# Kernel tuning notes

Hardware: AMD Instinct MI355X
Metric: run time of the kernel (lower is better)

## Reference

```python
import jax, jax.numpy as jnp
import numpy as np

GRID_SIZE = 5
SPLINE_ORDER = 3
HIDDEN = 128
IN_FT = 768
BATCH = 32768

def make_grid():
    # uniform grid on [-1, 1] extended by spline_order knots on each side
    h = 2.0 / GRID_SIZE
    return (jnp.arange(-SPLINE_ORDER, GRID_SIZE + SPLINE_ORDER + 1, dtype=jnp.float32) * h - 1.0)

def b_splines(x, grid):
    # x: (B, in) -> bases: (B, in, GRID_SIZE + SPLINE_ORDER) via Cox-de-Boor recursion
    xe = x[..., None]                                  # (B, in, 1)
    bases = ((xe >= grid[:-1]) & (xe < grid[1:])).astype(x.dtype)
    for k in range(1, SPLINE_ORDER + 1):
        left = (xe - grid[:-(k + 1)]) / (grid[k:-1] - grid[:-(k + 1)]) * bases[..., :-1]
        right = (grid[k + 1:] - xe) / (grid[k + 1:] - grid[1:-k]) * bases[..., 1:]
        bases = left + right
    return bases

def kan_layer(x, base_w, spline_w, grid):
    # base_w: (out, in); spline_w: (out, in, G+k)
    B = x.shape[0]
    base_out = jax.nn.silu(x) @ base_w.T
    bas = b_splines(x, grid).reshape(B, -1)            # (B, in*(G+k))
    spline_out = bas @ spline_w.reshape(spline_w.shape[0], -1).T
    return base_out + spline_out

def setup_inputs() -> dict:
    key = jax.random.key(0)
    ks = jax.random.split(key, 8)
    nb = GRID_SIZE + SPLINE_ORDER  # 8 basis functions per edge
    return {
        "stm": jax.random.uniform(ks[0], (BATCH, IN_FT), dtype=jnp.float32),
        "nstm": jax.random.uniform(ks[1], (BATCH, IN_FT), dtype=jnp.float32),
        "ft_w": jax.random.normal(ks[2], (HIDDEN, IN_FT), dtype=jnp.float32) * 0.02,
        "ft_b": jnp.zeros((HIDDEN,), dtype=jnp.float32),
        "kan1_base_w": jax.random.normal(ks[3], (HIDDEN, 2 * HIDDEN), dtype=jnp.float32) * 0.05,
        "kan1_spline_w": jax.random.normal(ks[4], (HIDDEN, 2 * HIDDEN, nb), dtype=jnp.float32) * 0.05,
        "kan2_base_w": jax.random.normal(ks[5], (1, HIDDEN), dtype=jnp.float32) * 0.05,
        "kan2_spline_w": jax.random.normal(ks[6], (1, HIDDEN, nb), dtype=jnp.float32) * 0.05,
    }

def reference(stm, nstm, ft_w, ft_b, kan1_base_w, kan1_spline_w, kan2_base_w, kan2_spline_w):
    grid = make_grid()
    stm_h = stm @ ft_w.T + ft_b
    nstm_h = nstm @ ft_w.T + ft_b
    hidden = jnp.concatenate([stm_h, nstm_h], axis=1)   # (B, 2*HIDDEN)
    hidden = kan_layer(hidden, kan1_base_w, kan1_spline_w, grid)
    out = kan_layer(hidden, kan2_base_w, kan2_spline_w, grid)
    return jax.nn.sigmoid(out)
```

## Files before the change

### kernel.cpp

```cpp
#include <hip/hip_runtime.h>
#include <hip/hip_bf16.h>
#include <math.h>
#include <stdint.h>

typedef __attribute__((ext_vector_type(8))) short bf16x8;
typedef __attribute__((ext_vector_type(4))) float f32x4;

__device__ __forceinline__ uint32_t pack2(float a, float b) {
    union { __hip_bfloat162 h2; uint32_t u; } c;
    c.h2 = __float22bfloat162_rn(make_float2(a, b));
    return c.u;
}
__device__ __forceinline__ unsigned short f2bf(float f) {
    union { __hip_bfloat16 h; unsigned short u; } c;
    c.h = __float2bfloat16(f);
    return c.u;
}
__device__ __forceinline__ float bf2f(unsigned short h) {
    union { uint32_t u; float f; } c; c.u = ((uint32_t)h) << 16;
    return c.f;
}
__device__ __forceinline__ float silu_f(float x) {
    return x / (1.0f + __expf(-x));
}

__device__ __forceinline__ void bspline8(float x, float* __restrict__ b) {
    const float tt = (x + 2.2f) * 2.5f;
#pragma unroll
    for (int v = 0; v < 8; ++v) {
        float y = fabsf(tt - (float)(v + 2));
        float p = fmaxf(2.0f - y, 0.0f);
        float q = fmaxf(1.0f - y, 0.0f);
        b[v] = (p * p * p - 4.0f * q * q * q) * (1.0f / 6.0f);
    }
}

__global__ __launch_bounds__(256) void prep_wbf(const float* __restrict__ ftw,
                                                unsigned short* __restrict__ WbF) {
    const int idx = blockIdx.x * 256 + threadIdx.x;
    const int e = idx & 7, l = (idx >> 3) & 63, ks = (idx >> 9) & 3;
    const int nt = (idx >> 11) & 1, wc = (idx >> 12) & 3, tile = idx >> 14;
    const int col = wc * 32 + nt * 16 + (l & 15);
    const int k = tile * 128 + ks * 32 + (l >> 4) * 8 + e;
    WbF[idx] = f2bf(ftw[(size_t)col * 768 + k]);
}

__global__ __launch_bounds__(256) void prep_bpf(const float* __restrict__ bw,
                                                const float* __restrict__ sw,
                                                unsigned short* __restrict__ BpF) {
    const int idx = blockIdx.x * 256 + threadIdx.x;
    const int e = idx & 7, l = (idx >> 3) & 63, ks = (idx >> 9) & 3;
    const int nt = (idx >> 11) & 1, wc = (idx >> 12) & 3, jb = idx >> 14;
    const int col = wc * 32 + nt * 16 + (l & 15);
    const int k = jb * 128 + ks * 32 + (l >> 4) * 8 + e;
    const int f = k >> 4, v = k & 15;
    float val = 0.f;
    if (v == 0) val = bw[col * 256 + f];
    else if (v <= 8) val = sw[(size_t)(col * 256 + f) * 8 + (v - 1)];
    BpF[idx] = f2bf(val);
}

__global__ __launch_bounds__(512, 4) void kan_fused(
        const float* __restrict__ stm, const float* __restrict__ nstm,
        const unsigned short* __restrict__ WbF, const float* __restrict__ bias,
        const unsigned short* __restrict__ BpF,
        const float* __restrict__ w2b, const float* __restrict__ w2s,
        float* __restrict__ out) {
    __shared__ alignas(16) char lds[65536];
    char* smA  = lds;
    char* phi1 = lds + 16384;
    char* smHT = lds + 32768;

    const int r0 = blockIdx.x * 64;
    const int t = threadIdx.x;
    const int l = t & 63, w = t >> 6;
    const int fr = l & 15, h = l >> 4;
    const int wr = w >> 2, wc = w & 3;

    const int arow = t >> 3;
    const int acol = (t & 7) * 16;
    const uint32_t adst0 = (uint32_t)arow * 256u +
        ((uint32_t)(((t & 7) * 2) ^ (arow & 15)) << 4);
    const uint32_t adst1 = (uint32_t)arow * 256u +
        ((uint32_t)(((t & 7) * 2 + 1) ^ (arow & 15)) << 4);

    f32x4 acc[2][2];
#pragma unroll
    for (int mt = 0; mt < 2; ++mt)
#pragma unroll
        for (int nt = 0; nt < 2; ++nt) acc[mt][nt] = (f32x4){0.f, 0.f, 0.f, 0.f};

    float4 regY[4], regZ[4];
    bf16x8 bf[2][4];

#define FT_ISSUE(REG, TK)                                                      \
    {                                                                          \
        const float* __restrict__ Ap = ((TK) >= 6) ? nstm : stm;               \
        const int kk = ((TK) % 6) * 128;                                       \
        _Pragma("unroll") for (int q = 0; q < 4; ++q)                          \
            REG[q] = *reinterpret_cast<const float4*>(                         \
                &Ap[(size_t)(r0 + arow) * 768 + kk + acol + q * 4]);           \
    }

#define FT_WRITE(REG)                                                          \
    {                                                                          \
        int4 w0, w1;                                                           \
        w0.x = (int)pack2(REG[0].x, REG[0].y);                                 \
        w0.y = (int)pack2(REG[0].z, REG[0].w);                                 \
        w0.z = (int)pack2(REG[1].x, REG[1].y);                                 \
        w0.w = (int)pack2(REG[1].z, REG[1].w);                                 \
        w1.x = (int)pack2(REG[2].x, REG[2].y);                                 \
        w1.y = (int)pack2(REG[2].z, REG[2].w);                                 \
        w1.z = (int)pack2(REG[3].x, REG[3].y);                                 \
        w1.w = (int)pack2(REG[3].z, REG[3].w);                                 \
        *reinterpret_cast<int4*>(smA + adst0) = w0;                            \
        *reinterpret_cast<int4*>(smA + adst1) = w1;                            \
    }

#define LOADF(PTR, TILE)                                                       \
    {                                                                          \
        const unsigned short* __restrict__ fb =                                \
            (PTR) + (size_t)(TILE) * 16384 + wc * 4096 + l * 8;                \
        _Pragma("unroll") for (int nt = 0; nt < 2; ++nt)                       \
            _Pragma("unroll") for (int ks = 0; ks < 4; ++ks)                   \
                bf[nt][ks] = *reinterpret_cast<const bf16x8*>(                 \
                    fb + nt * 2048 + ks * 512);                                \
    }

#define GEMM_STEP(PHI)                                                         \
    _Pragma("unroll") for (int ks = 0; ks < 4; ++ks) {                         \
        bf16x8 a[2];                                                           \
        _Pragma("unroll") for (int mt = 0; mt < 2; ++mt) {                     \
            const uint32_t row = (uint32_t)(wr * 32 + mt * 16 + fr);           \
            a[mt] = *reinterpret_cast<const bf16x8*>(                          \
                (PHI) + row * 256u +                                           \
                (((uint32_t)(ks * 4 + h) ^ (row & 15u)) << 4));                \
        }                                                                      \
        _Pragma("unroll") for (int mt = 0; mt < 2; ++mt)                       \
            _Pragma("unroll") for (int nt = 0; nt < 2; ++nt)                   \
                acc[mt][nt] = __builtin_amdgcn_mfma_f32_16x16x32_bf16(         \
                    a[mt], bf[nt][ks], acc[mt][nt], 0, 0, 0);                  \
    }

#define DUMP_H(SO)                                                             \
    _Pragma("unroll") for (int nt = 0; nt < 2; ++nt) {                         \
        const int col = wc * 32 + nt * 16 + fr;                                \
        const float bv = bias[col];                                            \
        const int feat = (SO) + col;                                           \
        _Pragma("unroll") for (int mt = 0; mt < 2; ++mt) {                     \
            const int rowb = wr * 32 + mt * 16 + h * 4;                        \
            int2 o;                                                            \
            o.x = (int)pack2(acc[mt][nt][0] + bv, acc[mt][nt][1] + bv);        \
            o.y = (int)pack2(acc[mt][nt][2] + bv, acc[mt][nt][3] + bv);        \
            const uint32_t db = (uint32_t)feat * 128u +                        \
                ((uint32_t)((rowb >> 3) ^ (feat & 7)) << 4) +                  \
                (uint32_t)(rowb & 7) * 2u;                                     \
            *reinterpret_cast<int2*>(smHT + db) = o;                           \
            acc[mt][nt] = (f32x4){0.f, 0.f, 0.f, 0.f};                         \
        }                                                                      \
    }

#define EXPAND(DST, JF)                                                        \
    {                                                                          \
        const int feat = (JF) * 8 + w;                                         \
        const unsigned short xv = *reinterpret_cast<const unsigned short*>(    \
            smHT + (uint32_t)feat * 128u +                                     \
            ((uint32_t)((l >> 3) ^ (feat & 7)) << 4) + (uint32_t)(l & 7) * 2u);\
        const float x = bf2f(xv);                                              \
        float bs[8];                                                           \
        bspline8(x, bs);                                                       \
        const uint32_t pw0 = pack2(silu_f(x), bs[0]);                          \
        const uint32_t pw1 = pack2(bs[1], bs[2]);                              \
        const uint32_t pw2 = pack2(bs[3], bs[4]);                              \
        const uint32_t pw3 = pack2(bs[5], bs[6]);                              \
        const uint32_t pw4 = pack2(bs[7], 0.f);                                \
        const uint32_t d0 = (uint32_t)l * 256u +                               \
            ((uint32_t)((2 * w) ^ (l & 15)) << 4);                             \
        const uint32_t d1 = (uint32_t)l * 256u +                               \
            ((uint32_t)((2 * w + 1) ^ (l & 15)) << 4);                         \
        *reinterpret_cast<int4*>((DST) + d0) =                                 \
            make_int4((int)pw0, (int)pw1, (int)pw2, (int)pw3);                 \
        *reinterpret_cast<int4*>((DST) + d1) = make_int4((int)pw4, 0, 0, 0);   \
    }

#define BAR1()                                                                 \
    asm volatile("s_waitcnt lgkmcnt(0)" ::: "memory");                         \
    __builtin_amdgcn_sched_barrier(0);                                         \
    __builtin_amdgcn_s_barrier();
#define BAR2()                                                                 \
    __builtin_amdgcn_sched_barrier(0);                                         \
    __builtin_amdgcn_s_barrier();                                              \
    __builtin_amdgcn_sched_barrier(0);

    FT_ISSUE(regY, 0);
    FT_ISSUE(regZ, 1);
#pragma unroll 1
    for (int pp = 0; pp < 6; ++pp) {
        FT_WRITE(regY);
        if (pp < 5) FT_ISSUE(regY, 2 * pp + 2);
        LOADF(WbF, (2 * pp) % 6);
        BAR1();
        __builtin_amdgcn_s_setprio(1);
        GEMM_STEP(smA);
        __builtin_amdgcn_s_setprio(0);
        BAR2();
        FT_WRITE(regZ);
        if (pp < 5) FT_ISSUE(regZ, 2 * pp + 3);
        LOADF(WbF, (2 * pp + 1) % 6);
        BAR1();
        __builtin_amdgcn_s_setprio(1);
        GEMM_STEP(smA);
        __builtin_amdgcn_s_setprio(0);
        if (pp == 2) { DUMP_H(0); }
        if (pp == 5) { DUMP_H(128); }
        asm volatile("s_waitcnt lgkmcnt(0)" ::: "memory");
        BAR2();
    }

    EXPAND(smA, 0);
#pragma unroll 1
    for (int jb = 0; jb < 32; ++jb) {
        char* phiC = (jb & 1) ? phi1 : smA;
        char* phiN = (jb & 1) ? smA : phi1;
        LOADF(BpF, jb);
        if (jb < 31) EXPAND(phiN, jb + 1);
        BAR1();
        __builtin_amdgcn_s_setprio(1);
        GEMM_STEP(phiC);
        __builtin_amdgcn_s_setprio(0);
        BAR2();
    }

    unsigned short* smH2 = (unsigned short*)lds;
#pragma unroll
    for (int mt = 0; mt < 2; ++mt)
#pragma unroll
        for (int nt = 0; nt < 2; ++nt) {
            const int col = wc * 32 + nt * 16 + fr;
#pragma unroll
            for (int j = 0; j < 4; ++j) {
                const int row = wr * 32 + mt * 16 + h * 4 + j;
                smH2[row * 136 + col] = f2bf(acc[mt][nt][j]);
            }
        }
    __syncthreads();
    const int row2 = t >> 3, qd = t & 7;
    float sum = 0.f;
#pragma unroll 4
    for (int i = 0; i < 16; ++i) {
        const int j = qd * 16 + ((i + qd * 2) & 15);
        const float x = bf2f(smH2[row2 * 136 + j]);
        float bs[8];
        bspline8(x, bs);
        const float4 s0 = *reinterpret_cast<const float4*>(&w2s[j * 8]);
        const float4 s1 = *reinterpret_cast<const float4*>(&w2s[j * 8 + 4]);
        float s = silu_f(x) * w2b[j];
        s += bs[0] * s0.x + bs[1] * s0.y + bs[2] * s0.z + bs[3] * s0.w;
        s += bs[4] * s1.x + bs[5] * s1.y + bs[6] * s1.z + bs[7] * s1.w;
        sum += s;
    }
    sum += __shfl_xor(sum, 1, 64);
    sum += __shfl_xor(sum, 2, 64);
    sum += __shfl_xor(sum, 4, 64);
    if (qd == 0) out[r0 + row2] = 1.0f / (1.0f + __expf(-sum));
}

extern "C" void kernel_launch(void* const* d_in, const int* in_sizes, int n_in,
                              void* d_out, int out_size, void* d_ws, size_t ws_size,
                              hipStream_t stream) {
    const float* stm  = (const float*)d_in[0];
    const float* nstm = (const float*)d_in[1];
    const float* ft_w = (const float*)d_in[2];
    const float* ft_b = (const float*)d_in[3];
    const float* k1bw = (const float*)d_in[4];
    const float* k1sw = (const float*)d_in[5];
    const float* k2bw = (const float*)d_in[6];
    const float* k2sw = (const float*)d_in[7];
    float* out = (float*)d_out;

    char* ws = (char*)d_ws;
    unsigned short* WbF = (unsigned short*)ws;
    unsigned short* BpF = (unsigned short*)(ws + 196608);

    prep_wbf<<<384, 256, 0, stream>>>(ft_w, WbF);
    prep_bpf<<<2048, 256, 0, stream>>>(k1bw, k1sw, BpF);
    kan_fused<<<512, 512, 0, stream>>>(stm, nstm, WbF, ft_b, BpF, k2bw, k2sw, out);
}
```

Measured before the change: 110.4 us.

## Warp-specialize fused KAN kernel into MFMA consumer and staging producer waves

The 8 waves are split into two roles. Four consumer waves each run a 32x64 output tile of MFMAs and prefetch the next weight fragments. Four producer waves stage the next A tile (bf16-converted input or B-spline expansion) into a double-buffered LDS slot. This replaces the old scheme in which all 8 waves alternated loading and computing, and aims to overlap global loads and spline expansion with matrix math using one barrier per step. The weight prep layouts are changed to match the 2x4 n-tiling. In exchange, half the waves now do no MFMA work, and each consumer needs more accumulator and fragment registers.

```diff
diff --git a/kernel.cpp b/kernel.cpp
--- a/kernel.cpp
+++ b/kernel.cpp
@@ -39,8 +39,8 @@
                                                 unsigned short* __restrict__ WbF) {
     const int idx = blockIdx.x * 256 + threadIdx.x;
     const int e = idx & 7, l = (idx >> 3) & 63, ks = (idx >> 9) & 3;
-    const int nt = (idx >> 11) & 1, wc = (idx >> 12) & 3, tile = idx >> 14;
-    const int col = wc * 32 + nt * 16 + (l & 15);
+    const int nt = (idx >> 11) & 3, wc = (idx >> 13) & 1, tile = idx >> 14;
+    const int col = wc * 64 + nt * 16 + (l & 15);
     const int k = tile * 128 + ks * 32 + (l >> 4) * 8 + e;
     WbF[idx] = f2bf(ftw[(size_t)col * 768 + k]);
 }
@@ -50,8 +50,8 @@
                                                 unsigned short* __restrict__ BpF) {
     const int idx = blockIdx.x * 256 + threadIdx.x;
     const int e = idx & 7, l = (idx >> 3) & 63, ks = (idx >> 9) & 3;
-    const int nt = (idx >> 11) & 1, wc = (idx >> 12) & 3, jb = idx >> 14;
-    const int col = wc * 32 + nt * 16 + (l & 15);
+    const int nt = (idx >> 11) & 3, wc = (idx >> 13) & 1, jb = idx >> 14;
+    const int col = wc * 64 + nt * 16 + (l & 15);
     const int k = jb * 128 + ks * 32 + (l >> 4) * 8 + e;
     const int f = k >> 4, v = k & 15;
     float val = 0.f;
@@ -67,84 +67,76 @@
         const float* __restrict__ w2b, const float* __restrict__ w2s,
         float* __restrict__ out) {
     __shared__ alignas(16) char lds[65536];
-    char* smA  = lds;
-    char* phi1 = lds + 16384;
+    char* buf0 = lds;
+    char* buf1 = lds + 16384;
     char* smHT = lds + 32768;
 
     const int r0 = blockIdx.x * 64;
     const int t = threadIdx.x;
     const int l = t & 63, w = t >> 6;
     const int fr = l & 15, h = l >> 4;
-    const int wr = w >> 2, wc = w & 3;
-
-    const int arow = t >> 3;
-    const int acol = (t & 7) * 16;
-    const uint32_t adst0 = (uint32_t)arow * 256u +
-        ((uint32_t)(((t & 7) * 2) ^ (arow & 15)) << 4);
-    const uint32_t adst1 = (uint32_t)arow * 256u +
-        ((uint32_t)(((t & 7) * 2 + 1) ^ (arow & 15)) << 4);
-
-    f32x4 acc[2][2];
+    const bool cons = (w < 4);
+    const int wr = (w >> 1) & 1, wc = w & 1;
+    const int p = w & 3;
+
+    f32x4 acc[2][4];
 #pragma unroll
     for (int mt = 0; mt < 2; ++mt)
 #pragma unroll
-        for (int nt = 0; nt < 2; ++nt) acc[mt][nt] = (f32x4){0.f, 0.f, 0.f, 0.f};
-
-    float4 regY[4], regZ[4];
-    bf16x8 bf[2][4];
-
-#define FT_ISSUE(REG, TK)                                                      \
-    {                                                                          \
-        const float* __restrict__ Ap = ((TK) >= 6) ? nstm : stm;               \
-        const int kk = ((TK) % 6) * 128;                                       \
-        _Pragma("unroll") for (int q = 0; q < 4; ++q)                          \
-            REG[q] = *reinterpret_cast<const float4*>(                         \
-                &Ap[(size_t)(r0 + arow) * 768 + kk + acol + q * 4]);           \
-    }
-
-#define FT_WRITE(REG)                                                          \
-    {                                                                          \
-        int4 w0, w1;                                                           \
-        w0.x = (int)pack2(REG[0].x, REG[0].y);                                 \
-        w0.y = (int)pack2(REG[0].z, REG[0].w);                                 \
-        w0.z = (int)pack2(REG[1].x, REG[1].y);                                 \
-        w0.w = (int)pack2(REG[1].z, REG[1].w);                                 \
-        w1.x = (int)pack2(REG[2].x, REG[2].y);                                 \
-        w1.y = (int)pack2(REG[2].z, REG[2].w);                                 \
-        w1.z = (int)pack2(REG[3].x, REG[3].y);                                 \
-        w1.w = (int)pack2(REG[3].z, REG[3].w);                                 \
-        *reinterpret_cast<int4*>(smA + adst0) = w0;                            \
-        *reinterpret_cast<int4*>(smA + adst1) = w1;                            \
-    }
+        for (int nt = 0; nt < 4; ++nt) acc[mt][nt] = (f32x4){0.f, 0.f, 0.f, 0.f};
+
+    bf16x8 bf[4][4];
 
 #define LOADF(PTR, TILE)                                                       \
     {                                                                          \
         const unsigned short* __restrict__ fb =                                \
-            (PTR) + (size_t)(TILE) * 16384 + wc * 4096 + l * 8;                \
-        _Pragma("unroll") for (int nt = 0; nt < 2; ++nt)                       \
+            (PTR) + (size_t)(TILE) * 16384 + wc * 8192 + l * 8;                \
+        _Pragma("unroll") for (int nt = 0; nt < 4; ++nt)                       \
             _Pragma("unroll") for (int ks = 0; ks < 4; ++ks)                   \
                 bf[nt][ks] = *reinterpret_cast<const bf16x8*>(                 \
                     fb + nt * 2048 + ks * 512);                                \
     }
 
-#define GEMM_STEP(PHI)                                                         \
+#define STAGE_A(DST, T)                                                        \
+    {                                                                          \
+        const float* __restrict__ Ap = ((T) >= 6) ? nstm : stm;                \
+        const int kk = ((T) % 6) * 128;                                        \
+        float4 fv[8];                                                          \
+        _Pragma("unroll") for (int i = 0; i < 8; ++i) {                        \
+            const int row = p * 16 + i * 2 + (l >> 5);                         \
+            fv[i] = *reinterpret_cast<const float4*>(                          \
+                &Ap[(size_t)(r0 + row) * 768 + kk + (l & 31) * 4]);            \
+        }                                                                      \
+        _Pragma("unroll") for (int i = 0; i < 8; ++i) {                        \
+            const int row = p * 16 + i * 2 + (l >> 5);                         \
+            const uint32_t c = (uint32_t)((l & 31) >> 1);                      \
+            const uint32_t dst = (uint32_t)row * 256u +                        \
+                ((c ^ (uint32_t)(row & 15)) << 4) + (uint32_t)(l & 1) * 8u;    \
+            int2 v;                                                            \
+            v.x = (int)pack2(fv[i].x, fv[i].y);                                \
+            v.y = (int)pack2(fv[i].z, fv[i].w);                                \
+            *reinterpret_cast<int2*>((DST) + dst) = v;                         \
+        }                                                                      \
+    }
+
+#define GEMM_STEP(SRC)                                                         \
     _Pragma("unroll") for (int ks = 0; ks < 4; ++ks) {                         \
         bf16x8 a[2];                                                           \
         _Pragma("unroll") for (int mt = 0; mt < 2; ++mt) {                     \
             const uint32_t row = (uint32_t)(wr * 32 + mt * 16 + fr);           \
             a[mt] = *reinterpret_cast<const bf16x8*>(                          \
-                (PHI) + row * 256u +                                           \
+                (SRC) + row * 256u +                                           \
                 (((uint32_t)(ks * 4 + h) ^ (row & 15u)) << 4));                \
         }                                                                      \
         _Pragma("unroll") for (int mt = 0; mt < 2; ++mt)                       \
-            _Pragma("unroll") for (int nt = 0; nt < 2; ++nt)                   \
+            _Pragma("unroll") for (int nt = 0; nt < 4; ++nt)                   \
                 acc[mt][nt] = __builtin_amdgcn_mfma_f32_16x16x32_bf16(         \
                     a[mt], bf[nt][ks], acc[mt][nt], 0, 0, 0);                  \
     }
 
 #define DUMP_H(SO)                                                             \
-    _Pragma("unroll") for (int nt = 0; nt < 2; ++nt) {                         \
-        const int col = wc * 32 + nt * 16 + fr;                                \
+    _Pragma("unroll") for (int nt = 0; nt < 4; ++nt) {                         \
+        const int col = wc * 64 + nt * 16 + fr;                                \
         const float bv = bias[col];                                            \
         const int feat = (SO) + col;                                           \
         _Pragma("unroll") for (int mt = 0; mt < 2; ++mt) {                     \
@@ -160,9 +152,10 @@
         }                                                                      \
     }
 
-#define EXPAND(DST, JF)                                                        \
-    {                                                                          \
-        const int feat = (JF) * 8 + w;                                         \
+#define EXPAND2(DST, JB)                                                       \
+    _Pragma("unroll") for (int e = 0; e < 2; ++e) {                            \
+        const int f = p * 2 + e;                                               \
+        const int feat = (JB) * 8 + f;                                         \
         const unsigned short xv = *reinterpret_cast<const unsigned short*>(    \
             smHT + (uint32_t)feat * 128u +                                     \
             ((uint32_t)((l >> 3) ^ (feat & 7)) << 4) + (uint32_t)(l & 7) * 2u);\
@@ -175,74 +168,72 @@
         const uint32_t pw3 = pack2(bs[5], bs[6]);                              \
         const uint32_t pw4 = pack2(bs[7], 0.f);                                \
         const uint32_t d0 = (uint32_t)l * 256u +                               \
-            ((uint32_t)((2 * w) ^ (l & 15)) << 4);                             \
+            ((uint32_t)((2 * f) ^ (l & 15)) << 4);                             \
         const uint32_t d1 = (uint32_t)l * 256u +                               \
-            ((uint32_t)((2 * w + 1) ^ (l & 15)) << 4);                         \
+            ((uint32_t)((2 * f + 1) ^ (l & 15)) << 4);                         \
         *reinterpret_cast<int4*>((DST) + d0) =                                 \
             make_int4((int)pw0, (int)pw1, (int)pw2, (int)pw3);                 \
         *reinterpret_cast<int4*>((DST) + d1) = make_int4((int)pw4, 0, 0, 0);   \
     }
 
-#define BAR1()                                                                 \
+#define PH_BAR()                                                               \
     asm volatile("s_waitcnt lgkmcnt(0)" ::: "memory");                         \
-    __builtin_amdgcn_sched_barrier(0);                                         \
-    __builtin_amdgcn_s_barrier();
-#define BAR2()                                                                 \
     __builtin_amdgcn_sched_barrier(0);                                         \
     __builtin_amdgcn_s_barrier();                                              \
     __builtin_amdgcn_sched_barrier(0);
 
-    FT_ISSUE(regY, 0);
-    FT_ISSUE(regZ, 1);
+    if (cons) { LOADF(WbF, 0); }
+    else      { STAGE_A(buf0, 0); }
+    PH_BAR();
 #pragma unroll 1
-    for (int pp = 0; pp < 6; ++pp) {
-        FT_WRITE(regY);
-        if (pp < 5) FT_ISSUE(regY, 2 * pp + 2);
-        LOADF(WbF, (2 * pp) % 6);
-        BAR1();
-        __builtin_amdgcn_s_setprio(1);
-        GEMM_STEP(smA);
-        __builtin_amdgcn_s_setprio(0);
-        BAR2();
-        FT_WRITE(regZ);
-        if (pp < 5) FT_ISSUE(regZ, 2 * pp + 3);
-        LOADF(WbF, (2 * pp + 1) % 6);
-        BAR1();
-        __builtin_amdgcn_s_setprio(1);
-        GEMM_STEP(smA);
-        __builtin_amdgcn_s_setprio(0);
-        if (pp == 2) { DUMP_H(0); }
-        if (pp == 5) { DUMP_H(128); }
-        asm volatile("s_waitcnt lgkmcnt(0)" ::: "memory");
-        BAR2();
-    }
-
-    EXPAND(smA, 0);
+    for (int tile = 0; tile < 12; ++tile) {
+        char* cur = (tile & 1) ? buf1 : buf0;
+        char* nxt = (tile & 1) ? buf0 : buf1;
+        if (cons) {
+            __builtin_amdgcn_s_setprio(1);
+            GEMM_STEP(cur);
+            __builtin_amdgcn_s_setprio(0);
+            if (tile < 11) { LOADF(WbF, (tile + 1) % 6); }
+            if (tile == 5) { DUMP_H(0); }
+            if (tile == 11) { DUMP_H(128); }
+        } else {
+            if (tile < 11) { STAGE_A(nxt, tile + 1); }
+        }
+        PH_BAR();
+    }
+
+    if (cons) { LOADF(BpF, 0); }
+    else      { EXPAND2(buf0, 0); }
+    PH_BAR();
 #pragma unroll 1
     for (int jb = 0; jb < 32; ++jb) {
-        char* phiC = (jb & 1) ? phi1 : smA;
-        char* phiN = (jb & 1) ? smA : phi1;
-        LOADF(BpF, jb);
-        if (jb < 31) EXPAND(phiN, jb + 1);
-        BAR1();
-        __builtin_amdgcn_s_setprio(1);
-        GEMM_STEP(phiC);
-        __builtin_amdgcn_s_setprio(0);
-        BAR2();
+        char* cur = (jb & 1) ? buf1 : buf0;
+        char* nxt = (jb & 1) ? buf0 : buf1;
+        if (cons) {
+            __builtin_amdgcn_s_setprio(1);
+            GEMM_STEP(cur);
+            __builtin_amdgcn_s_setprio(0);
+            if (jb < 31) { LOADF(BpF, jb + 1); }
+        } else {
+            if (jb < 31) { EXPAND2(nxt, jb + 1); }
+        }
+        PH_BAR();
     }
 
     unsigned short* smH2 = (unsigned short*)lds;
-#pragma unroll
-    for (int mt = 0; mt < 2; ++mt)
-#pragma unroll
-        for (int nt = 0; nt < 2; ++nt) {
-            const int col = wc * 32 + nt * 16 + fr;
-#pragma unroll
-            for (int j = 0; j < 4; ++j) {
-                const int row = wr * 32 + mt * 16 + h * 4 + j;
-                smH2[row * 136 + col] = f2bf(acc[mt][nt][j]);
+    if (cons) {
+#pragma unroll
+        for (int mt = 0; mt < 2; ++mt)
+#pragma unroll
+            for (int nt = 0; nt < 4; ++nt) {
+                const int col = wc * 64 + nt * 16 + fr;
+#pragma unroll
+                for (int j = 0; j < 4; ++j) {
+                    const int row = wr * 32 + mt * 16 + h * 4 + j;
+                    smH2[row * 136 + col] = f2bf(acc[mt][nt][j]);
+                }
             }
-        }
+    }
     __syncthreads();
     const int row2 = t >> 3, qd = t & 7;
     float sum = 0.f;
```

Result: slower. 363.9 us (+229.7%).
